# Kernel optimization log

Hardware: AMD Instinct MI355X
Metric: run time of the kernel (lower is better)

## Reference

```python
import jax, jax.numpy as jnp
import numpy as np

B, H, L = 16, 256, 4096
C, KD, NS = 1, 32, 8  # channels, kernel_dim, num_scales


def _interp_linear(k, s):
    """torch F.interpolate(mode='linear', align_corners=False) with integer scale s.
    k: (C, H, Lin) -> (C, H, Lin*s)."""
    if s == 1:
        return k
    Lin = k.shape[-1]
    x = (jnp.arange(Lin * s, dtype=jnp.float32) + 0.5) / s - 0.5
    x = jnp.clip(x, 0.0, Lin - 1)
    x0 = jnp.floor(x).astype(jnp.int32)
    x1 = jnp.minimum(x0 + 1, Lin - 1)
    w = (x - x0.astype(jnp.float32)).astype(k.dtype)
    return k[..., x0] * (1.0 - w) + k[..., x1] * w


def _build_kernel(kernels):
    # multiplier = linspace(decay_min=2, decay_max=2, H) -> all 2.0, shape (1,H,1)
    multiplier = jnp.linspace(2.0, 2.0, H).reshape(1, H, 1)
    parts = []
    for i in range(NS):
        s = 2 ** max(0, i - 1)  # init_scale = 0
        parts.append(_interp_linear(kernels[i], s) * multiplier ** (NS - i - 1))
    return jnp.concatenate(parts, axis=-1)  # (C, H, 4096)


def setup_inputs() -> dict:
    key = jax.random.key(0)
    k0, k1, k2, k3, k4 = jax.random.split(key, 5)
    u = jax.random.normal(k0, (B, H, L), jnp.float32)
    kernels = jax.random.normal(k1, (NS, C, H, KD), jnp.float32)
    D = jax.random.normal(k2, (C, H), jnp.float32)
    W_out = jax.random.normal(k3, (H, C * H), jnp.float32) * 0.05
    b_out = jax.random.normal(k4, (H,), jnp.float32) * 0.05
    return {"u": u, "kernels": kernels, "D": D, "W_out": W_out, "b_out": b_out}


def reference(u, kernels, D, W_out, b_out):
    k = _build_kernel(kernels)  # (C, H, Lk)
    Lk = k.shape[-1]
    if Lk > L:
        k = k[..., :L]
    elif Lk < L:
        k = jnp.pad(k, ((0, 0), (0, 0), (0, L - Lk)))
    # kernel_norm is detached on first forward
    norm = jax.lax.stop_gradient(jnp.linalg.norm(k, axis=-1, keepdims=True))
    k = k / norm
    n = 2 * L
    k_f = jnp.fft.rfft(k, n=n)  # (C, H, L+1) complex
    u_f = jnp.fft.rfft(u, n=n)  # (B, H, L+1) complex
    y_f = jnp.einsum('bhl,chl->bchl', u_f, k_f)
    y = jnp.fft.irfft(y_f, n=n)[..., :L]  # (B, C, H, L)
    y = y + jnp.einsum('bhl,ch->bchl', u, D)
    y = y.reshape(B, C * H, L)
    y = jax.nn.gelu(y, approximate=False)  # nn.GELU exact
    y = jnp.transpose(y, (0, 2, 1))  # (B, L, C*H)
    y = y @ W_out.T + b_out  # output_linear: C*H -> H
    return jnp.transpose(y, (0, 2, 1))  # (B, H, L)
```

## Files before the change

kernel.cpp:

```cpp
#include <hip/hip_runtime.h>


#define C1f 0.92387953251128674f
#define S1f 0.38268343236508977f
#define C2f 0.70710678118654752f

typedef __attribute__((ext_vector_type(8))) short bf16x8;
typedef __attribute__((ext_vector_type(4))) float f32x4;

static __device__ __forceinline__ unsigned short f2bf(float f) {
  unsigned u = __float_as_uint(f);
  u += 0x7FFFu + ((u >> 16) & 1u);
  return (unsigned short)(u >> 16);
}

static __device__ __forceinline__ void cmul(float& ar, float& ai, float br, float bi) {
  float t = ar * br - ai * bi;
  ai = ar * bi + ai * br;
  ar = t;
}

static __device__ __forceinline__ float gelu_t(float x) {
  float x2 = x * x;
  float t = x * __builtin_fmaf(0.044715f, x2, 1.f);
  float e = __expf(-1.5957691216f * t);
  return x / (1.f + e);
}

__device__ __constant__ float W32C[16] = {
  1.f, 0.98078528040323044913f, 0.92387953251128675613f, 0.83146961230254523708f,
  0.70710678118654752440f, 0.55557023301960222474f, 0.38268343236508977173f,
  0.19509032201612826785f, 0.f, -0.19509032201612826785f, -0.38268343236508977173f,
  -0.55557023301960222474f, -0.70710678118654752440f, -0.83146961230254523708f,
  -0.92387953251128675613f, -0.98078528040323044913f};
__device__ __constant__ float W32S[16] = {
  0.f, 0.19509032201612826785f, 0.38268343236508977173f, 0.55557023301960222474f,
  0.70710678118654752440f, 0.83146961230254523708f, 0.92387953251128675613f,
  0.98078528040323044913f, 1.f, 0.98078528040323044913f, 0.92387953251128675613f,
  0.83146961230254523708f, 0.70710678118654752440f, 0.55557023301960222474f,
  0.38268343236508977173f, 0.19509032201612826785f};

static __device__ __forceinline__ void dft16_fwd(float* xr, float* xi) {
  const float wr[8] = {1.f, C1f, C2f, S1f, 0.f, -S1f, -C2f, -C1f};
  const float wi[8] = {0.f, -S1f, -C2f, -C1f, -1.f, -C1f, -C2f, -S1f};
#pragma unroll
  for (int j = 0; j < 8; ++j) {
    float ar = xr[j], ai = xi[j], br = xr[j + 8], bi = xi[j + 8];
    xr[j] = ar + br; xi[j] = ai + bi;
    float dr = ar - br, di = ai - bi;
    xr[j + 8] = dr * wr[j] - di * wi[j];
    xi[j + 8] = dr * wi[j] + di * wr[j];
  }
#pragma unroll
  for (int h = 0; h < 2; ++h) {
#pragma unroll
    for (int j = 0; j < 4; ++j) {
      int i0 = h * 8 + j, i1 = i0 + 4;
      float ar = xr[i0], ai = xi[i0], br = xr[i1], bi = xi[i1];
      xr[i0] = ar + br; xi[i0] = ai + bi;
      float dr = ar - br, di = ai - bi;
      xr[i1] = dr * wr[2 * j] - di * wi[2 * j];
      xi[i1] = dr * wi[2 * j] + di * wr[2 * j];
    }
  }
#pragma unroll
  for (int h = 0; h < 4; ++h) {
    int base = h * 4;
    {
      int i0 = base, i1 = base + 2;
      float ar = xr[i0], ai = xi[i0], br = xr[i1], bi = xi[i1];
      xr[i0] = ar + br; xi[i0] = ai + bi;
      xr[i1] = ar - br; xi[i1] = ai - bi;
    }
    {
      int i0 = base + 1, i1 = base + 3;
      float ar = xr[i0], ai = xi[i0], br = xr[i1], bi = xi[i1];
      xr[i0] = ar + br; xi[i0] = ai + bi;
      float dr = ar - br, di = ai - bi;
      xr[i1] = di; xi[i1] = -dr;
    }
  }
#pragma unroll
  for (int h = 0; h < 8; ++h) {
    int i0 = h * 2, i1 = i0 + 1;
    float ar = xr[i0], ai = xi[i0], br = xr[i1], bi = xi[i1];
    xr[i0] = ar + br; xi[i0] = ai + bi;
    xr[i1] = ar - br; xi[i1] = ai - bi;
  }
}

template <bool HALF>
static __device__ __forceinline__ void dft16_inv_t(float* xr, float* xi) {
  const float wr[8] = {1.f, C1f, C2f, S1f, 0.f, -S1f, -C2f, -C1f};
  const float wi[8] = {0.f, S1f, C2f, C1f, 1.f, C1f, C2f, S1f};
#pragma unroll
  for (int h = 0; h < 8; ++h) {
    int i0 = h * 2, i1 = i0 + 1;
    float ar = xr[i0], ai = xi[i0], br = xr[i1], bi = xi[i1];
    xr[i0] = ar + br; xi[i0] = ai + bi;
    xr[i1] = ar - br; xi[i1] = ai - bi;
  }
#pragma unroll
  for (int h = 0; h < 4; ++h) {
    int base = h * 4;
    {
      int i0 = base, i1 = base + 2;
      float ar = xr[i0], ai = xi[i0], tr = xr[i1], ti = xi[i1];
      xr[i0] = ar + tr; xi[i0] = ai + ti;
      xr[i1] = ar - tr; xi[i1] = ai - ti;
    }
    {
      int i0 = base + 1, i1 = base + 3;
      float ar = xr[i0], ai = xi[i0], br = xr[i1], bi = xi[i1];
      float tr = -bi, ti = br;
      xr[i0] = ar + tr; xi[i0] = ai + ti;
      xr[i1] = ar - tr; xi[i1] = ai - ti;
    }
  }
#pragma unroll
  for (int h = 0; h < 2; ++h) {
#pragma unroll
    for (int j = 0; j < 4; ++j) {
      int i0 = h * 8 + j, i1 = i0 + 4;
      float br = xr[i1], bi = xi[i1];
      float tr = br * wr[2 * j] - bi * wi[2 * j];
      float ti = br * wi[2 * j] + bi * wr[2 * j];
      float ar = xr[i0], ai = xi[i0];
      xr[i0] = ar + tr; xi[i0] = ai + ti;
      xr[i1] = ar - tr; xi[i1] = ai - ti;
    }
  }
#pragma unroll
  for (int j = 0; j < 8; ++j) {
    int i0 = j, i1 = j + 8;
    float br = xr[i1], bi = xi[i1];
    float tr = br * wr[j] - bi * wi[j];
    float ti = br * wi[j] + bi * wr[j];
    float ar = xr[i0], ai = xi[i0];
    xr[i0] = ar + tr; xi[i0] = ai + ti;
    if (!HALF) { xr[i1] = ar - tr; xi[i1] = ai - ti; }
  }
}

#define REV_INIT constexpr int REV[16] = {0, 8, 4, 12, 2, 10, 6, 14, 1, 9, 5, 13, 3, 11, 7, 15}

#define TWCHAIN(XR, XI, CR, CI)                         \
  {                                                     \
    float pr_ = (CR), pi_ = (CI);                       \
    cmul(XR[8], XI[8], pr_, pi_);                       \
    _Pragma("unroll") for (int k = 2; k < 16; ++k) {    \
      cmul(pr_, pi_, (CR), (CI));                       \
      cmul(XR[REV[k]], XI[REV[k]], pr_, pi_);           \
    }                                                   \
  }


static __device__ __forceinline__ void fft8192_fwd(float* xr, float* xi, float* lbuf,
                                                   int t, const float2* __restrict__ tw) {
  REV_INIT;
  int bs1 = t + (t >> 5);
  int bg1 = ((t >> 5) << 9) + (t & 31) + ((t >> 5) << 4);
  int qq = t & 1;
  int bg2 = 33 * (t >> 1) + qq;
  dft16_fwd(xr, xi);
  {
    float2 w1 = tw[t];
    TWCHAIN(xr, xi, w1.x, w1.y);
  }
#pragma unroll
  for (int j = 0; j < 16; ++j) lbuf[bs1 + 528 * REV[j]] = xr[j];
  __syncthreads();
#pragma unroll
  for (int m = 0; m < 16; ++m) xr[m] = lbuf[bg1 + 33 * m];
  __syncthreads();
#pragma unroll
  for (int j = 0; j < 16; ++j) lbuf[bs1 + 528 * REV[j]] = xi[j];
  __syncthreads();
#pragma unroll
  for (int m = 0; m < 16; ++m) xi[m] = lbuf[bg1 + 33 * m];
  dft16_fwd(xr, xi);
  {
    float2 w1 = tw[(t & 31) << 4];
    TWCHAIN(xr, xi, w1.x, w1.y);
  }
#pragma unroll
  for (int j = 0; j < 16; ++j) lbuf[bg1 + 33 * REV[j]] = xr[j];
  __syncthreads();
#pragma unroll
  for (int m = 0; m < 16; ++m) xr[m] = lbuf[bg2 + 2 * m];
  __syncthreads();
#pragma unroll
  for (int j = 0; j < 16; ++j) lbuf[bg1 + 33 * REV[j]] = xi[j];
  __syncthreads();
#pragma unroll
  for (int m = 0; m < 16; ++m) xi[m] = lbuf[bg2 + 2 * m];
  dft16_fwd(xr, xi);
  if (qq) {
#pragma unroll
    for (int k = 1; k < 16; ++k) cmul(xr[REV[k]], xi[REV[k]], W32C[k], -W32S[k]);
  }
  float sgn = qq ? -1.f : 1.f;
#pragma unroll
  for (int j = 0; j < 16; ++j) {
    float pr = __shfl_xor(xr[j], 1);
    float pi = __shfl_xor(xi[j], 1);
    xr[j] = sgn * xr[j] + pr;
    xi[j] = sgn * xi[j] + pi;
  }
}

static __device__ __forceinline__ void fft8192_inv(float* xr, float* xi, float* lbuf,
                                                   int t, const float2* __restrict__ tw) {
  REV_INIT;
  int bs1 = t + (t >> 5);
  int bg1 = ((t >> 5) << 9) + (t & 31) + ((t >> 5) << 4);
  int qq = t & 1;
  int bg2 = 33 * (t >> 1) + qq;
  float sgn = qq ? -1.f : 1.f;
#pragma unroll
  for (int j = 0; j < 16; ++j) {
    float pr = __shfl_xor(xr[j], 1);
    float pi = __shfl_xor(xi[j], 1);
    xr[j] = sgn * xr[j] + pr;
    xi[j] = sgn * xi[j] + pi;
  }
  if (qq) {
#pragma unroll
    for (int k = 1; k < 16; ++k) cmul(xr[REV[k]], xi[REV[k]], W32C[k], W32S[k]);
  }
  dft16_inv_t<false>(xr, xi);
#pragma unroll
  for (int m = 0; m < 16; ++m) lbuf[bg2 + 2 * m] = xr[m];
  __syncthreads();
#pragma unroll
  for (int j = 0; j < 16; ++j) xr[j] = lbuf[bg1 + 33 * REV[j]];
  __syncthreads();
#pragma unroll
  for (int m = 0; m < 16; ++m) lbuf[bg2 + 2 * m] = xi[m];
  __syncthreads();
#pragma unroll
  for (int j = 0; j < 16; ++j) xi[j] = lbuf[bg1 + 33 * REV[j]];
  {
    float2 w1 = tw[(t & 31) << 4];
    TWCHAIN(xr, xi, w1.x, -w1.y);
  }
  dft16_inv_t<false>(xr, xi);
#pragma unroll
  for (int m = 0; m < 16; ++m) lbuf[bg1 + 33 * m] = xr[m];
  __syncthreads();
#pragma unroll
  for (int j = 0; j < 16; ++j) xr[j] = lbuf[bs1 + 528 * REV[j]];
  __syncthreads();
#pragma unroll
  for (int m = 0; m < 16; ++m) lbuf[bg1 + 33 * m] = xi[m];
  __syncthreads();
#pragma unroll
  for (int j = 0; j < 16; ++j) xi[j] = lbuf[bs1 + 528 * REV[j]];
  {
    float2 w1 = tw[t];
    TWCHAIN(xr, xi, w1.x, -w1.y);
  }
  dft16_inv_t<true>(xr, xi);
}

__global__ void __launch_bounds__(256) gconv_setup(
    const float* __restrict__ kernels,
    const float* __restrict__ W_out,
    float* __restrict__ k_norm,
    float2* __restrict__ tw,
    unsigned short* __restrict__ Wbf)
{
  int blk = blockIdx.x;
  int tid = threadIdx.x;
  if (blk < 256) {
    int h = blk;
    __shared__ float red[256];
    float val[16];
    float ss = 0.0f;
#pragma unroll
    for (int r = 0; r < 16; ++r) {
      int l = tid + 256 * r;
      int i;
      if (l < 32) i = 0;
      else if (l < 64) i = 1;
      else i = (31 - __clz(l)) - 4;
      int off = (i == 0) ? 0 : (16 << i);
      int s = (i <= 1) ? 1 : (1 << (i - 1));
      float mult = (float)(1 << (7 - i));
      int j = l - off;
      const float* kb = kernels + ((size_t)i * 256 + h) * 32;
      float v;
      if (s == 1) {
        v = kb[j];
      } else {
        float x = ((float)j + 0.5f) / (float)s - 0.5f;
        x = fminf(fmaxf(x, 0.0f), 31.0f);
        float xf = floorf(x);
        int x0 = (int)xf;
        int x1 = min(x0 + 1, 31);
        float w = x - xf;
        v = kb[x0] * (1.0f - w) + kb[x1] * w;
      }
      v *= mult;
      val[r] = v;
      ss += v * v;
    }
    red[tid] = ss;
    __syncthreads();
    for (int o = 128; o > 0; o >>= 1) {
      if (tid < o) red[tid] += red[tid + o];
      __syncthreads();
    }
    float inv = 1.0f / sqrtf(red[0]);
#pragma unroll
    for (int r = 0; r < 16; ++r)
      k_norm[(size_t)h * 4096 + tid + 256 * r] = val[r] * inv;
  } else if (blk < 258) {
    int idx = (blk - 256) * 256 + tid;
    double ang = -6.283185307179586477 * (double)idx / 8192.0;
    tw[idx] = make_float2((float)cos(ang), (float)sin(ang));
  } else {
    int o = (blk - 258) * 256 + tid;
    Wbf[o] = f2bf(W_out[o]);
  }
}

__global__ void __launch_bounds__(512, 4) gconv_kfft(
    const float* __restrict__ k_norm,
    const float* __restrict__ Dvec,
    const float2* __restrict__ tw,
    float2* __restrict__ Kst)
{
  __shared__ float lbuf[8448];
  int h = blockIdx.x;
  int t = threadIdx.x;
  float xr[16], xi[16];
  const float* kn = k_norm + ((size_t)h << 12);
#pragma unroll
  for (int m = 0; m < 8; ++m) { xr[m] = kn[t + (m << 9)]; xi[m] = 0.f; }
#pragma unroll
  for (int m = 8; m < 16; ++m) { xr[m] = 0.f; xi[m] = 0.f; }
  fft8192_fwd(xr, xi, lbuf, t, tw);
  float Dh = Dvec[h];
  const float sc = 1.0f / 8192.0f;
  float2* out = Kst + ((size_t)h << 13) + (t << 4);
#pragma unroll
  for (int j = 0; j < 16; ++j)
    out[j] = make_float2((xr[j] + Dh) * sc, xi[j] * sc);
}

__global__ void __launch_bounds__(512, 4) gconv_main(
    const float* __restrict__ u,
    const float2* __restrict__ tw,
    const float2* __restrict__ Kst,
    unsigned short* __restrict__ g)
{
  __shared__ float lbuf[8448];
  int blk = blockIdx.x;
  int h = blk & 255;
  int pb = blk >> 8;
  int t = threadIdx.x;
  const float* u0 = u + ((size_t)(pb * 256 + h) << 12);
  const float* u1 = u + ((size_t)((pb + 8) * 256 + h) << 12);
  float xr[16], xi[16];
#pragma unroll
  for (int m = 0; m < 8; ++m) { xr[m] = u0[t + (m << 9)]; xi[m] = u1[t + (m << 9)]; }
#pragma unroll
  for (int m = 8; m < 16; ++m) { xr[m] = 0.f; xi[m] = 0.f; }
  fft8192_fwd(xr, xi, lbuf, t, tw);
  const float2* kr = Kst + ((size_t)h << 13) + (t << 4);
#pragma unroll
  for (int j = 0; j < 16; ++j) {
    float2 kv = kr[j];
    cmul(xr[j], xi[j], kv.x, kv.y);
  }
  fft8192_inv(xr, xi, lbuf, t, tw);
  unsigned short* g0 = g + ((size_t)(pb * 256 + h) << 12) + t;
  unsigned short* g1 = g + ((size_t)((pb + 8) * 256 + h) << 12) + t;
#pragma unroll
  for (int m = 0; m < 8; ++m) {
    g0[m << 9] = f2bf(gelu_t(xr[m]));
    g1[m << 9] = f2bf(gelu_t(xi[m]));
  }
}

__global__ void __launch_bounds__(256) gconv_out(
    const unsigned short* __restrict__ g,
    const unsigned short* __restrict__ Wbf,
    const float* __restrict__ b_out,
    float* __restrict__ out)
{
  __shared__ unsigned short As[128][40];
  __shared__ unsigned short Bs[32][132];
  int l0 = blockIdx.x * 128;
  int m0 = blockIdx.y * 128;
  int b  = blockIdx.z;
  int tid = threadIdx.x;
  int lane = tid & 63, wid = tid >> 6;
  int wm = (wid >> 1) * 64, wl = (wid & 1) * 64;
  int lhi = lane >> 4, llo = lane & 15;
  f32x4 acc[4][4];
#pragma unroll
  for (int a = 0; a < 4; ++a)
#pragma unroll
    for (int c = 0; c < 4; ++c) acc[a][c] = (f32x4){0.f, 0.f, 0.f, 0.f};

  for (int ks = 0; ks < 8; ++ks) {
    int k0 = ks * 32;
#pragma unroll
    for (int i = 0; i < 2; ++i) {
      int idx = tid + i * 256;
      int m = idx >> 2, c = idx & 3;
      *(uint4*)&As[m][c * 8] =
          *(const uint4*)(Wbf + ((size_t)(m0 + m) << 8) + k0 + c * 8);
      int k = idx >> 4, cc = idx & 15;
      const unsigned short* gp =
          g + ((size_t)(b * 256 + k0 + k) << 12) + l0 + cc * 8;
      ((uint2*)&Bs[k][cc * 8])[0] = ((const uint2*)gp)[0];
      ((uint2*)&Bs[k][cc * 8])[1] = ((const uint2*)gp)[1];
    }
    __syncthreads();
    int kk = lhi * 8;
    bf16x8 af[4], bfr[4];
#pragma unroll
    for (int f = 0; f < 4; ++f)
      af[f] = *(bf16x8*)&As[wm + f * 16 + llo][kk];
#pragma unroll
    for (int f = 0; f < 4; ++f) {
      bf16x8 v;
#pragma unroll
      for (int j = 0; j < 8; ++j)
        v[j] = (short)Bs[kk + j][wl + f * 16 + llo];
      bfr[f] = v;
    }
#pragma unroll
    for (int fm = 0; fm < 4; ++fm)
#pragma unroll
      for (int fl = 0; fl < 4; ++fl)
        acc[fm][fl] = __builtin_amdgcn_mfma_f32_16x16x32_bf16(
            af[fm], bfr[fl], acc[fm][fl], 0, 0, 0);
    __syncthreads();
  }
#pragma unroll
  for (int fm = 0; fm < 4; ++fm) {
#pragma unroll
    for (int r = 0; r < 4; ++r) {
      int m = m0 + wm + fm * 16 + lhi * 4 + r;
      float bias = b_out[m];
      float* op = out + ((size_t)(b * 256 + m) << 12) + l0 + wl + llo;
#pragma unroll
      for (int fl = 0; fl < 4; ++fl)
        op[fl * 16] = acc[fm][fl][r] + bias;
    }
  }
}

extern "C" void kernel_launch(void* const* d_in, const int* in_sizes, int n_in,
                              void* d_out, int out_size, void* d_ws, size_t ws_size,
                              hipStream_t stream) {
  (void)in_sizes; (void)n_in; (void)out_size; (void)ws_size;
  const float* u       = (const float*)d_in[0];
  const float* kernels = (const float*)d_in[1];
  const float* Dvec    = (const float*)d_in[2];
  const float* W_out   = (const float*)d_in[3];
  const float* b_out   = (const float*)d_in[4];
  float* out = (float*)d_out;
  char* ws = (char*)d_ws;

  float*  k_norm = (float*)(ws);
  float2* tw     = (float2*)(ws + (4u << 20));
  unsigned short* Wbf = (unsigned short*)(ws + (4u << 20) + (128u << 10));
  float2* Kst    = (float2*)(ws + (8u << 20));
  unsigned short* g = (unsigned short*)(ws + (24u << 20));

  gconv_setup<<<514, 256, 0, stream>>>(kernels, W_out, k_norm, tw, Wbf);
  gconv_kfft<<<256, 512, 0, stream>>>(k_norm, Dvec, tw, Kst);
  gconv_main<<<2048, 512, 0, stream>>>(u, tw, Kst, g);
  dim3 gd(32, 2, 16);
  gconv_out<<<gd, 256, 0, stream>>>(g, Wbf, b_out, out);
}
```

Baseline: 112.0 us.

## Redesign FFT shared-memory transposes with float4 scatter and unpadded strided gather

Replaces the padded, bit-reversed scalar shared-memory exchange in the 8192-point forward and inverse FFT with a layout where each thread writes its 16 values as four float4 stores and reads back with a stride of 512. Twiddle indexing and the final-stage index mapping change to match the new data ordering, and the shared buffer shrinks from 8448 to 8192 floats. The aim is fewer LDS instructions and a smaller LDS footprint. The risk is bank conflicts on the float4 stores, since each thread's stride of 16 floats is no longer padded. GELU also swaps a division for a hardware reciprocal.

```diff
diff --git a/kernel.cpp b/kernel.cpp
--- a/kernel.cpp
+++ b/kernel.cpp
@@ -24,7 +24,7 @@
   float x2 = x * x;
   float t = x * __builtin_fmaf(0.044715f, x2, 1.f);
   float e = __expf(-1.5957691216f * t);
-  return x / (1.f + e);
+  return x * __builtin_amdgcn_rcpf(1.f + e);
 }
 
 __device__ __constant__ float W32C[16] = {
@@ -155,51 +155,56 @@
   }
 
 
+#define SCATQ(XX)                                                   \
+  {                                                                 \
+    float4* qp_ = (float4*)(lbuf + 16 * t);                         \
+    qp_[0] = make_float4(XX[0], XX[8], XX[4], XX[12]);              \
+    qp_[1] = make_float4(XX[2], XX[10], XX[6], XX[14]);             \
+    qp_[2] = make_float4(XX[1], XX[9], XX[5], XX[13]);              \
+    qp_[3] = make_float4(XX[3], XX[11], XX[7], XX[15]);             \
+  }
+#define GATHQ(XX)                                                   \
+  {                                                                 \
+    const float4* qp_ = (const float4*)(lbuf + 16 * t);             \
+    float4 v0_ = qp_[0], v1_ = qp_[1], v2_ = qp_[2], v3_ = qp_[3];  \
+    XX[0] = v0_.x; XX[8] = v0_.y; XX[4] = v0_.z; XX[12] = v0_.w;    \
+    XX[2] = v1_.x; XX[10] = v1_.y; XX[6] = v1_.z; XX[14] = v1_.w;   \
+    XX[1] = v2_.x; XX[9] = v2_.y; XX[5] = v2_.z; XX[13] = v2_.w;    \
+    XX[3] = v3_.x; XX[11] = v3_.y; XX[7] = v3_.z; XX[15] = v3_.w;   \
+  }
+#define GATHS(XX, BASE)                                             \
+  _Pragma("unroll") for (int m_ = 0; m_ < 16; ++m_) XX[m_] = lbuf[(BASE) + 512 * m_];
+#define SCATS(XX, BASE)                                             \
+  _Pragma("unroll") for (int m_ = 0; m_ < 16; ++m_) lbuf[(BASE) + 512 * m_] = XX[m_];
+
 static __device__ __forceinline__ void fft8192_fwd(float* xr, float* xi, float* lbuf,
                                                    int t, const float2* __restrict__ tw) {
   REV_INIT;
-  int bs1 = t + (t >> 5);
-  int bg1 = ((t >> 5) << 9) + (t & 31) + ((t >> 5) << 4);
-  int qq = t & 1;
-  int bg2 = 33 * (t >> 1) + qq;
+  int vb2 = (t >> 1) + 256 * (t & 1);
   dft16_fwd(xr, xi);
   {
     float2 w1 = tw[t];
     TWCHAIN(xr, xi, w1.x, w1.y);
   }
-#pragma unroll
-  for (int j = 0; j < 16; ++j) lbuf[bs1 + 528 * REV[j]] = xr[j];
-  __syncthreads();
-#pragma unroll
-  for (int m = 0; m < 16; ++m) xr[m] = lbuf[bg1 + 33 * m];
-  __syncthreads();
-#pragma unroll
-  for (int j = 0; j < 16; ++j) lbuf[bs1 + 528 * REV[j]] = xi[j];
-  __syncthreads();
-#pragma unroll
-  for (int m = 0; m < 16; ++m) xi[m] = lbuf[bg1 + 33 * m];
+  SCATQ(xr); __syncthreads();
+  GATHS(xr, t); __syncthreads();
+  SCATQ(xi); __syncthreads();
+  GATHS(xi, t); __syncthreads();
   dft16_fwd(xr, xi);
   {
-    float2 w1 = tw[(t & 31) << 4];
+    float2 w1 = tw[(t >> 4) << 4];
     TWCHAIN(xr, xi, w1.x, w1.y);
   }
-#pragma unroll
-  for (int j = 0; j < 16; ++j) lbuf[bg1 + 33 * REV[j]] = xr[j];
-  __syncthreads();
-#pragma unroll
-  for (int m = 0; m < 16; ++m) xr[m] = lbuf[bg2 + 2 * m];
-  __syncthreads();
-#pragma unroll
-  for (int j = 0; j < 16; ++j) lbuf[bg1 + 33 * REV[j]] = xi[j];
-  __syncthreads();
-#pragma unroll
-  for (int m = 0; m < 16; ++m) xi[m] = lbuf[bg2 + 2 * m];
+  SCATQ(xr); __syncthreads();
+  GATHS(xr, vb2); __syncthreads();
+  SCATQ(xi); __syncthreads();
+  GATHS(xi, vb2);
   dft16_fwd(xr, xi);
-  if (qq) {
+  if (t & 1) {
 #pragma unroll
     for (int k = 1; k < 16; ++k) cmul(xr[REV[k]], xi[REV[k]], W32C[k], -W32S[k]);
   }
-  float sgn = qq ? -1.f : 1.f;
+  float sgn = (t & 1) ? -1.f : 1.f;
 #pragma unroll
   for (int j = 0; j < 16; ++j) {
     float pr = __shfl_xor(xr[j], 1);
@@ -212,11 +217,8 @@
 static __device__ __forceinline__ void fft8192_inv(float* xr, float* xi, float* lbuf,
                                                    int t, const float2* __restrict__ tw) {
   REV_INIT;
-  int bs1 = t + (t >> 5);
-  int bg1 = ((t >> 5) << 9) + (t & 31) + ((t >> 5) << 4);
-  int qq = t & 1;
-  int bg2 = 33 * (t >> 1) + qq;
-  float sgn = qq ? -1.f : 1.f;
+  int vb2 = (t >> 1) + 256 * (t & 1);
+  float sgn = (t & 1) ? -1.f : 1.f;
 #pragma unroll
   for (int j = 0; j < 16; ++j) {
     float pr = __shfl_xor(xr[j], 1);
@@ -224,38 +226,26 @@
     xr[j] = sgn * xr[j] + pr;
     xi[j] = sgn * xi[j] + pi;
   }
-  if (qq) {
+  if (t & 1) {
 #pragma unroll
     for (int k = 1; k < 16; ++k) cmul(xr[REV[k]], xi[REV[k]], W32C[k], W32S[k]);
   }
   dft16_inv_t<false>(xr, xi);
-#pragma unroll
-  for (int m = 0; m < 16; ++m) lbuf[bg2 + 2 * m] = xr[m];
   __syncthreads();
-#pragma unroll
-  for (int j = 0; j < 16; ++j) xr[j] = lbuf[bg1 + 33 * REV[j]];
+  SCATS(xr, vb2); __syncthreads();
+  GATHQ(xr); __syncthreads();
+  SCATS(xi, vb2); __syncthreads();
+  GATHQ(xi);
+  {
+    float2 w1 = tw[(t >> 4) << 4];
+    TWCHAIN(xr, xi, w1.x, -w1.y);
+  }
+  dft16_inv_t<false>(xr, xi);
   __syncthreads();
-#pragma unroll
-  for (int m = 0; m < 16; ++m) lbuf[bg2 + 2 * m] = xi[m];
-  __syncthreads();
-#pragma unroll
-  for (int j = 0; j < 16; ++j) xi[j] = lbuf[bg1 + 33 * REV[j]];
-  {
-    float2 w1 = tw[(t & 31) << 4];
-    TWCHAIN(xr, xi, w1.x, -w1.y);
-  }
-  dft16_inv_t<false>(xr, xi);
-#pragma unroll
-  for (int m = 0; m < 16; ++m) lbuf[bg1 + 33 * m] = xr[m];
-  __syncthreads();
-#pragma unroll
-  for (int j = 0; j < 16; ++j) xr[j] = lbuf[bs1 + 528 * REV[j]];
-  __syncthreads();
-#pragma unroll
-  for (int m = 0; m < 16; ++m) lbuf[bg1 + 33 * m] = xi[m];
-  __syncthreads();
-#pragma unroll
-  for (int j = 0; j < 16; ++j) xi[j] = lbuf[bs1 + 528 * REV[j]];
+  SCATS(xr, t); __syncthreads();
+  GATHQ(xr); __syncthreads();
+  SCATS(xi, t); __syncthreads();
+  GATHQ(xi);
   {
     float2 w1 = tw[t];
     TWCHAIN(xr, xi, w1.x, -w1.y);
@@ -331,7 +321,7 @@
     const float2* __restrict__ tw,
     float2* __restrict__ Kst)
 {
-  __shared__ float lbuf[8448];
+  __shared__ float lbuf[8192];
   int h = blockIdx.x;
   int t = threadIdx.x;
   float xr[16], xi[16];
@@ -355,7 +345,7 @@
     const float2* __restrict__ Kst,
     unsigned short* __restrict__ g)
 {
-  __shared__ float lbuf[8448];
+  __shared__ float lbuf[8192];
   int blk = blockIdx.x;
   int h = blk & 255;
   int pb = blk >> 8;
```

Result: slower. 140.3 us (+25.2%).
